# Performance work log

Measured on AMD Instinct MI355X. Metric: run time of the kernel, lower is better.

The kernel has to match this reference:

```python
import jax, jax.numpy as jnp
import numpy as np

D_MODEL = 1024
NUM_HEADS = 16
THETA = 10000.0


def setup_inputs() -> dict:
    key = jax.random.key(0)
    ks = jax.random.split(key, 5)
    B, S, DM = 4, 2048, D_MODEL
    std = 2.0 / (DM + DM)
    return {
        "x": jax.random.normal(ks[0], (B, S, DM), dtype=jnp.float32),
        "w_q": jax.random.normal(ks[1], (DM, DM), dtype=jnp.float32) * std,
        "w_k": jax.random.normal(ks[2], (DM, DM), dtype=jnp.float32) * std,
        "w_v": jax.random.normal(ks[3], (DM, DM), dtype=jnp.float32) * std,
        "w_o": jax.random.normal(ks[4], (DM, DM), dtype=jnp.float32) * std,
        "token_positions": jnp.arange(S, dtype=jnp.int64 if jax.config.jax_enable_x64 else jnp.int32),
    }


def _apply_rope(t, pos, d_k):
    # t: (b, h, s, d_k); pos: (s,)
    half = d_k // 2
    k = jnp.arange(half, dtype=jnp.float32)
    inv_freq = THETA ** (-2.0 * k / d_k)          # (half,)
    ang = pos.astype(jnp.float32)[:, None] * inv_freq  # (s, half)
    cos, sin = jnp.cos(ang), jnp.sin(ang)
    xe = t[..., 0::2]  # (b, h, s, half)
    xo = t[..., 1::2]
    re = cos * xe - sin * xo
    ro = sin * xe + cos * xo
    return jnp.stack([re, ro], axis=-1).reshape(t.shape)


def reference(x, w_q, w_k, w_v, w_o, token_positions):
    B, S, DM = x.shape
    H = NUM_HEADS
    d = DM // H
    # projections: x @ W.T, W is (h*d, d_model)
    def proj(w):
        y = jnp.einsum('bsm,em->bse', x, w)
        return y.reshape(B, S, H, d).transpose(0, 2, 1, 3)  # (b, h, s, d)
    q, k, v = proj(w_q), proj(w_k), proj(w_v)
    q = _apply_rope(q, token_positions, d)
    k = _apply_rope(k, token_positions, d)
    scale = 1.0 / jnp.sqrt(jnp.float32(d))
    scores = jnp.einsum('bhqd,bhkd->bhqk', q, k) * scale  # (b, h, s, s)
    causal = jnp.tril(jnp.ones((S, S), dtype=bool))
    scores = jnp.where(causal, scores, -jnp.inf)
    attn = jax.nn.softmax(scores, axis=-1)
    out = jnp.einsum('bhqk,bhkd->bhqd', attn, v)
    out = out.transpose(0, 2, 1, 3).reshape(B, S, DM)
    return jnp.einsum('bse,oe->bso', out, w_o)
```

## Files before the change

### kernel.cpp

```cpp
#include <hip/hip_runtime.h>
#include <hip/hip_bf16.h>

typedef __attribute__((ext_vector_type(8))) __bf16 bf16x8;
typedef __attribute__((ext_vector_type(2))) __bf16 bf16x2;
typedef __attribute__((ext_vector_type(2))) float f32x2;
typedef __attribute__((ext_vector_type(4))) float f32x4;
typedef __attribute__((ext_vector_type(16))) float f32x16;
typedef __attribute__((ext_vector_type(4))) unsigned int u32x4;
typedef __attribute__((ext_vector_type(2))) int i32x2;

#define MFMA16 __builtin_amdgcn_mfma_f32_16x16x32_bf16
#define MFMA32 __builtin_amdgcn_mfma_f32_32x32x16_bf16
#define GLOAD_LDS(g, l)                                                      \
  __builtin_amdgcn_global_load_lds(                                          \
      (const __attribute__((address_space(1))) void*)(g),                    \
      (__attribute__((address_space(3))) void*)(l), 16, 0, 0)

static __device__ __forceinline__ unsigned short f2bf(float f) {
  return __builtin_bit_cast(unsigned short, (__bf16)f);
}
static __device__ __forceinline__ unsigned int cvt2(float a, float b) {
  f32x2 t = {a, b};
  return __builtin_bit_cast(unsigned int, __builtin_convertvector(t, bf16x2));
}

__global__ __launch_bounds__(256) void cast_bf16_k(const float* __restrict__ in,
                                                   unsigned short* __restrict__ out,
                                                   int n8) {
  int i = blockIdx.x * 256 + threadIdx.x;
  if (i >= n8) return;
  const float4* p = (const float4*)in + (size_t)i * 2;
  float4 a = p[0], b = p[1];
  uint4 r;
  r.x = cvt2(a.x, a.y); r.y = cvt2(a.z, a.w);
  r.z = cvt2(b.x, b.y); r.w = cvt2(b.z, b.w);
  *((uint4*)out + i) = r;
}

__global__ __launch_bounds__(256) void rope_tab_k(const int* __restrict__ pos,
                                                  float2* __restrict__ tab) {
  int t = blockIdx.x * 256 + threadIdx.x;
  int s = t >> 5, k = t & 31;
  float p = (float)pos[s];
  float inv = powf(10000.0f, -(float)(2 * k) / 64.0f);
  float ang = p * inv;
  tab[t] = make_float2(cosf(ang), sinf(ang));
}

template <int MODE>
__global__ __launch_bounds__(256) void gemm_bt(
    const unsigned short* __restrict__ A, const unsigned short* __restrict__ W,
    unsigned short* __restrict__ Qb, unsigned short* __restrict__ Kb,
    unsigned short* __restrict__ Vb, float* __restrict__ Cout,
    const float2* __restrict__ rtab) {
  __shared__ unsigned short As[128 * 64];
  __shared__ unsigned short Bs[128 * 64];
  const int tid = threadIdx.x;
  const int lane = tid & 63;
  const int w = tid >> 6;
  const int wr = w >> 1, wc = w & 1;
  const int hi = lane >> 4, lo = lane & 15;
  const int m0 = blockIdx.x * 128;
  const int n0 = blockIdx.y * 128;
  const int z = blockIdx.z;
  const unsigned short* Bmat = W + (size_t)z * 1024 * 1024;

  const int sr = lane >> 3;
  const int sc8 = (lane & 7) * 8;

  f32x4 acc[4][4] = {};

  for (int kt = 0; kt < 16; ++kt) {
    const int kofs = kt * 64;
#pragma unroll
    for (int c = 0; c < 4; ++c) {
      const int rowA = c * 32 + w * 8;
      const unsigned short* ga = A + (size_t)(m0 + rowA + sr) * 1024 + kofs + sc8;
      GLOAD_LDS(ga, &As[rowA * 64]);
      const unsigned short* gb = Bmat + (size_t)(n0 + rowA + sr) * 1024 + kofs + sc8;
      GLOAD_LDS(gb, &Bs[rowA * 64]);
    }
    __syncthreads();
#pragma unroll
    for (int kb = 0; kb < 2; ++kb) {
      bf16x8 af[4], bfr[4];
#pragma unroll
      for (int mt = 0; mt < 4; ++mt)
        af[mt] = *(const bf16x8*)&As[(wr * 64 + mt * 16 + lo) * 64 + kb * 32 + hi * 8];
#pragma unroll
      for (int nt = 0; nt < 4; ++nt)
        bfr[nt] = *(const bf16x8*)&Bs[(wc * 64 + nt * 16 + lo) * 64 + kb * 32 + hi * 8];
#pragma unroll
      for (int mt = 0; mt < 4; ++mt)
#pragma unroll
        for (int nt = 0; nt < 4; ++nt)
          acc[mt][nt] = MFMA16(af[mt], bfr[nt], acc[mt][nt], 0, 0, 0);
    }
    __syncthreads();
  }

#pragma unroll
  for (int mt = 0; mt < 4; ++mt) {
#pragma unroll
    for (int nt = 0; nt < 4; ++nt) {
      const int c = n0 + wc * 64 + nt * 16 + lo;
#pragma unroll
      for (int j = 0; j < 4; ++j) {
        const int r = m0 + wr * 64 + mt * 16 + hi * 4 + j;
        float v = acc[mt][nt][j];
        if constexpr (MODE == 1) {
          Cout[(size_t)r * 1024 + c] = v;
        } else if constexpr (MODE == 2) {
          Vb[(size_t)r * 8192 + c] = f2bf(v);
        } else {
          const float other = __shfl_xor(v, 1);
          const int b = r >> 11, s = r & 2047;
          const int h = c >> 6, dd = c & 63;
          float2 cs = rtab[s * 32 + (dd >> 1)];
          float outv = (dd & 1) ? (cs.y * other + cs.x * v)
                                : (cs.x * v - cs.y * other);
          if (z == 0) outv *= 0.18033688012f;
          unsigned short* dst = (z == 0) ? Qb : Kb;
          dst[((size_t)(b * 16 + h) * 2048 + s) * 64 + dd] = f2bf(outv);
        }
      }
    }
  }
}

__global__ __launch_bounds__(256) void attn_k(const unsigned short* __restrict__ Qb,
                                              const unsigned short* __restrict__ Kb,
                                              const unsigned short* __restrict__ VtG,
                                              unsigned short* __restrict__ Ob) {
  __shared__ unsigned short Kl[2][64 * 64];
  __shared__ unsigned short Vl[2][64 * 64];
  const int tid = threadIdx.x;
  const int lane = tid & 63;
  const int w = tid >> 6;
  const int q32 = lane & 31;
  const int hi = lane >> 5;
  const int l7 = lane & 7;
  const int lin = blockIdx.x;
  const int slot = lin >> 3;
  const int bh = (lin & 7) * 8 + (slot >> 3);
  const int p = slot & 7;
  const int b = bh >> 4, h = bh & 15;
  const unsigned short* Qp = Qb + (size_t)bh * 2048 * 64;
  const unsigned short* Kp = Kb + (size_t)bh * 2048 * 64;
  const unsigned short* Vg = VtG + (size_t)h * 64 * 8192 + b * 2048;

  const int srow = lane >> 3;
  const int csrc = l7 ^ srow;

  auto stage = [&](int kt, int buf) {
#pragma unroll
    for (int i = 0; i < 2; ++i) {
      const int r = w * 16 + i * 8 + srow;
      GLOAD_LDS(Kp + ((size_t)(kt * 64 + r)) * 64 + csrc * 8,
                &Kl[buf][(w * 16 + i * 8) * 64]);
      GLOAD_LDS(Vg + (size_t)r * 8192 + kt * 64 + csrc * 8,
                &Vl[buf][(w * 16 + i * 8) * 64]);
    }
  };

  for (int phase = 0; phase < 2; ++phase) {
    const int qt = phase ? p : 15 - p;
    const int qw = qt * 128 + w * 32;
    const int qpos = qw + q32;

    bf16x8 qf[4];
#pragma unroll
    for (int ds = 0; ds < 4; ++ds)
      qf[ds] = *(const bf16x8*)&Qp[(size_t)qpos * 64 + ds * 16 + hi * 8];

    f32x16 oa0 = {}, oa1 = {};
    float mrow = -1e30f, lsum = 0.0f;
    const int ntiles = 2 * qt + 2;

    stage(0, 0);
    asm volatile("s_waitcnt vmcnt(0)" ::: "memory");
    __builtin_amdgcn_s_barrier();
    asm volatile("" ::: "memory");

    int cur = 0;
    for (int kt = 0; kt < ntiles; ++kt) {
      if (kt + 1 < ntiles) stage(kt + 1, cur ^ 1);
      const unsigned short* Kc = &Kl[cur][0];
      const unsigned short* Vc = &Vl[cur][0];

      f32x16 s0 = {}, s1 = {};
#pragma unroll
      for (int ds = 0; ds < 4; ++ds) {
        const int cc = ((ds * 2 + hi) ^ l7) * 8;
        bf16x8 k0 = *(const bf16x8*)&Kc[q32 * 64 + cc];
        bf16x8 k1 = *(const bf16x8*)&Kc[(32 + q32) * 64 + cc];
        s0 = MFMA32(k0, qf[ds], s0, 0, 0, 0);
        s1 = MFMA32(k1, qf[ds], s1, 0, 0, 0);
      }

      if (kt * 64 + 63 > qw) {
#pragma unroll
        for (int r = 0; r < 16; ++r) {
          const int krel = (r & 3) + 8 * (r >> 2) + 4 * hi;
          if (kt * 64 + krel > qpos) s0[r] = -1e30f;
          if (kt * 64 + 32 + krel > qpos) s1[r] = -1e30f;
        }
      }

      float tmax = -1e30f;
#pragma unroll
      for (int r = 0; r < 16; ++r) tmax = fmaxf(tmax, fmaxf(s0[r], s1[r]));
      tmax = fmaxf(tmax, __shfl_xor(tmax, 32));
      if (!__all(tmax - mrow <= 8.0f)) {
        const float mnew = fmaxf(mrow, tmax);
        const float alpha = exp2f(mrow - mnew);
        mrow = mnew;
        lsum *= alpha;
#pragma unroll
        for (int r = 0; r < 16; ++r) { oa0[r] *= alpha; oa1[r] *= alpha; }
      }
      float rsum = 0.0f;
#pragma unroll
      for (int r = 0; r < 16; ++r) {
        s0[r] = exp2f(s0[r] - mrow);
        s1[r] = exp2f(s1[r] - mrow);
        rsum += s0[r] + s1[r];
      }
      rsum += __shfl_xor(rsum, 32);
      lsum += rsum;

      unsigned int A0[8], A1[8];
#pragma unroll
      for (int i = 0; i < 8; ++i) {
        A0[i] = cvt2(s0[2 * i], s0[2 * i + 1]);
        A1[i] = cvt2(s1[2 * i], s1[2 * i + 1]);
      }
      i32x2 r02 = __builtin_amdgcn_permlane32_swap((int)A0[0], (int)A0[2], 0, 0);
      i32x2 r13 = __builtin_amdgcn_permlane32_swap((int)A0[1], (int)A0[3], 0, 0);
      i32x2 r46 = __builtin_amdgcn_permlane32_swap((int)A0[4], (int)A0[6], 0, 0);
      i32x2 r57 = __builtin_amdgcn_permlane32_swap((int)A0[5], (int)A0[7], 0, 0);
      i32x2 t02 = __builtin_amdgcn_permlane32_swap((int)A1[0], (int)A1[2], 0, 0);
      i32x2 t13 = __builtin_amdgcn_permlane32_swap((int)A1[1], (int)A1[3], 0, 0);
      i32x2 t46 = __builtin_amdgcn_permlane32_swap((int)A1[4], (int)A1[6], 0, 0);
      i32x2 t57 = __builtin_amdgcn_permlane32_swap((int)A1[5], (int)A1[7], 0, 0);
      const u32x4 pw0 = {(unsigned)r02[0], (unsigned)r13[0], (unsigned)r02[1], (unsigned)r13[1]};
      const u32x4 pw1 = {(unsigned)r46[0], (unsigned)r57[0], (unsigned)r46[1], (unsigned)r57[1]};
      const u32x4 pw2 = {(unsigned)t02[0], (unsigned)t13[0], (unsigned)t02[1], (unsigned)t13[1]};
      const u32x4 pw3 = {(unsigned)t46[0], (unsigned)t57[0], (unsigned)t46[1], (unsigned)t57[1]};

#pragma unroll
      for (int ks = 0; ks < 4; ++ks) {
        const int cc = ((ks * 2 + hi) ^ l7) * 8;
        bf16x8 v0 = *(const bf16x8*)&Vc[q32 * 64 + cc];
        bf16x8 v1 = *(const bf16x8*)&Vc[(32 + q32) * 64 + cc];
        const u32x4 pwk = (ks == 0) ? pw0 : (ks == 1) ? pw1 : (ks == 2) ? pw2 : pw3;
        bf16x8 pb = __builtin_bit_cast(bf16x8, pwk);
        oa0 = MFMA32(v0, pb, oa0, 0, 0, 0);
        oa1 = MFMA32(v1, pb, oa1, 0, 0, 0);
      }

      asm volatile("s_waitcnt vmcnt(0)" ::: "memory");
      __builtin_amdgcn_s_barrier();
      asm volatile("" ::: "memory");
      cur ^= 1;
    }

    const float invl = 1.0f / lsum;
    unsigned short* orow = Ob + ((size_t)(b * 2048 + qpos)) * 1024 + h * 64;
#pragma unroll
    for (int g = 0; g < 4; ++g) {
      uint2 o0, o1;
      o0.x = cvt2(oa0[4 * g + 0] * invl, oa0[4 * g + 1] * invl);
      o0.y = cvt2(oa0[4 * g + 2] * invl, oa0[4 * g + 3] * invl);
      o1.x = cvt2(oa1[4 * g + 0] * invl, oa1[4 * g + 1] * invl);
      o1.y = cvt2(oa1[4 * g + 2] * invl, oa1[4 * g + 3] * invl);
      *(uint2*)&orow[g * 8 + hi * 4] = o0;
      *(uint2*)&orow[32 + g * 8 + hi * 4] = o1;
    }
  }
}

extern "C" void kernel_launch(void* const* d_in, const int* in_sizes, int n_in,
                              void* d_out, int out_size, void* d_ws, size_t ws_size,
                              hipStream_t stream) {
  const float* x  = (const float*)d_in[0];
  const float* wq = (const float*)d_in[1];
  const float* wk = (const float*)d_in[2];
  const float* wv = (const float*)d_in[3];
  const float* wo = (const float*)d_in[4];
  const int* pos  = (const int*)d_in[5];

  char* ws = (char*)d_ws;
  unsigned short* xb  = (unsigned short*)(ws);
  unsigned short* wb  = (unsigned short*)(ws + 16777216);
  unsigned short* Qb  = (unsigned short*)(ws + 25165824);
  unsigned short* Kb  = (unsigned short*)(ws + 41943040);
  unsigned short* Vt  = (unsigned short*)(ws + 58720256);
  unsigned short* Ob  = (unsigned short*)(ws + 75497472);
  float2* tab         = (float2*)(ws + 92274688);

  cast_bf16_k<<<4096, 256, 0, stream>>>(x, xb, 1048576);
  cast_bf16_k<<<512, 256, 0, stream>>>(wq, wb + 0 * 1048576, 131072);
  cast_bf16_k<<<512, 256, 0, stream>>>(wk, wb + 1 * 1048576, 131072);
  cast_bf16_k<<<512, 256, 0, stream>>>(wv, wb + 2 * 1048576, 131072);
  cast_bf16_k<<<512, 256, 0, stream>>>(wo, wb + 3 * 1048576, 131072);
  rope_tab_k<<<256, 256, 0, stream>>>(pos, tab);
  gemm_bt<0><<<dim3(64, 8, 2), 256, 0, stream>>>(xb, wb, Qb, Kb, nullptr, nullptr, tab);
  gemm_bt<2><<<dim3(8, 64, 1), 256, 0, stream>>>(wb + 2 * 1048576, xb, nullptr,
                                                 nullptr, Vt, nullptr, tab);
  attn_k<<<dim3(512), 256, 0, stream>>>(Qb, Kb, Vt, Ob);
  gemm_bt<1><<<dim3(64, 8, 1), 256, 0, stream>>>(Ob, wb + 3 * 1048576, nullptr,
                                                 nullptr, nullptr, (float*)d_out, tab);
}
```

Before: 305.7 us.

## Switch projection GEMM to 32x32 MFMA with XOR-swizzled LDS layout

Replaces the 16x16x32 MFMA tiling in the projection/output GEMM with 32x32x16 MFMAs (four 32x32 accumulators per wave). The global-to-LDS loads now write chunks in an XOR-swizzled column order that matches the fragment reads, to avoid LDS bank conflicts. The aim is fewer LDS fragment reads per MFMA and higher MFMA throughput. The epilogue row mapping is rewritten to follow the 32x32 accumulator layout.

```diff
diff --git a/kernel.cpp b/kernel.cpp
--- a/kernel.cpp
+++ b/kernel.cpp
@@ -4,12 +4,10 @@
 typedef __attribute__((ext_vector_type(8))) __bf16 bf16x8;
 typedef __attribute__((ext_vector_type(2))) __bf16 bf16x2;
 typedef __attribute__((ext_vector_type(2))) float f32x2;
-typedef __attribute__((ext_vector_type(4))) float f32x4;
 typedef __attribute__((ext_vector_type(16))) float f32x16;
 typedef __attribute__((ext_vector_type(4))) unsigned int u32x4;
 typedef __attribute__((ext_vector_type(2))) int i32x2;
 
-#define MFMA16 __builtin_amdgcn_mfma_f32_16x16x32_bf16
 #define MFMA32 __builtin_amdgcn_mfma_f32_32x32x16_bf16
 #define GLOAD_LDS(g, l)                                                      \
   __builtin_amdgcn_global_load_lds(                                          \
@@ -59,62 +57,63 @@
   const int lane = tid & 63;
   const int w = tid >> 6;
   const int wr = w >> 1, wc = w & 1;
-  const int hi = lane >> 4, lo = lane & 15;
+  const int q32 = lane & 31;
+  const int hi = lane >> 5;
+  const int l7 = lane & 7;
   const int m0 = blockIdx.x * 128;
   const int n0 = blockIdx.y * 128;
   const int z = blockIdx.z;
   const unsigned short* Bmat = W + (size_t)z * 1024 * 1024;
 
   const int sr = lane >> 3;
-  const int sc8 = (lane & 7) * 8;
-
-  f32x4 acc[4][4] = {};
+  const int csrc = l7 ^ sr;
+
+  f32x16 acc00 = {}, acc01 = {}, acc10 = {}, acc11 = {};
 
   for (int kt = 0; kt < 16; ++kt) {
     const int kofs = kt * 64;
 #pragma unroll
     for (int c = 0; c < 4; ++c) {
       const int rowA = c * 32 + w * 8;
-      const unsigned short* ga = A + (size_t)(m0 + rowA + sr) * 1024 + kofs + sc8;
-      GLOAD_LDS(ga, &As[rowA * 64]);
-      const unsigned short* gb = Bmat + (size_t)(n0 + rowA + sr) * 1024 + kofs + sc8;
-      GLOAD_LDS(gb, &Bs[rowA * 64]);
+      GLOAD_LDS(A + (size_t)(m0 + rowA + sr) * 1024 + kofs + csrc * 8,
+                &As[rowA * 64]);
+      GLOAD_LDS(Bmat + (size_t)(n0 + rowA + sr) * 1024 + kofs + csrc * 8,
+                &Bs[rowA * 64]);
     }
     __syncthreads();
 #pragma unroll
-    for (int kb = 0; kb < 2; ++kb) {
-      bf16x8 af[4], bfr[4];
-#pragma unroll
-      for (int mt = 0; mt < 4; ++mt)
-        af[mt] = *(const bf16x8*)&As[(wr * 64 + mt * 16 + lo) * 64 + kb * 32 + hi * 8];
-#pragma unroll
-      for (int nt = 0; nt < 4; ++nt)
-        bfr[nt] = *(const bf16x8*)&Bs[(wc * 64 + nt * 16 + lo) * 64 + kb * 32 + hi * 8];
-#pragma unroll
-      for (int mt = 0; mt < 4; ++mt)
-#pragma unroll
-        for (int nt = 0; nt < 4; ++nt)
-          acc[mt][nt] = MFMA16(af[mt], bfr[nt], acc[mt][nt], 0, 0, 0);
+    for (int kk = 0; kk < 4; ++kk) {
+      const int cc = ((kk * 2 + hi) ^ l7) * 8;
+      bf16x8 a0 = *(const bf16x8*)&As[(wr * 64 + q32) * 64 + cc];
+      bf16x8 a1 = *(const bf16x8*)&As[(wr * 64 + 32 + q32) * 64 + cc];
+      bf16x8 b0 = *(const bf16x8*)&Bs[(wc * 64 + q32) * 64 + cc];
+      bf16x8 b1 = *(const bf16x8*)&Bs[(wc * 64 + 32 + q32) * 64 + cc];
+      acc00 = MFMA32(a0, b0, acc00, 0, 0, 0);
+      acc01 = MFMA32(a0, b1, acc01, 0, 0, 0);
+      acc10 = MFMA32(a1, b0, acc10, 0, 0, 0);
+      acc11 = MFMA32(a1, b1, acc11, 0, 0, 0);
     }
     __syncthreads();
   }
 
 #pragma unroll
-  for (int mt = 0; mt < 4; ++mt) {
-#pragma unroll
-    for (int nt = 0; nt < 4; ++nt) {
-      const int c = n0 + wc * 64 + nt * 16 + lo;
-#pragma unroll
-      for (int j = 0; j < 4; ++j) {
-        const int r = m0 + wr * 64 + mt * 16 + hi * 4 + j;
-        float v = acc[mt][nt][j];
+  for (int mt = 0; mt < 2; ++mt) {
+#pragma unroll
+    for (int nt = 0; nt < 2; ++nt) {
+      const f32x16 av = (mt == 0) ? (nt == 0 ? acc00 : acc01)
+                                  : (nt == 0 ? acc10 : acc11);
+      const int c = n0 + wc * 64 + nt * 32 + q32;
+#pragma unroll
+      for (int r = 0; r < 16; ++r) {
+        const int rr = m0 + wr * 64 + mt * 32 + (r & 3) + 8 * (r >> 2) + 4 * hi;
+        float v = av[r];
         if constexpr (MODE == 1) {
-          Cout[(size_t)r * 1024 + c] = v;
+          Cout[(size_t)rr * 1024 + c] = v;
         } else if constexpr (MODE == 2) {
-          Vb[(size_t)r * 8192 + c] = f2bf(v);
+          Vb[(size_t)rr * 8192 + c] = f2bf(v);
         } else {
           const float other = __shfl_xor(v, 1);
-          const int b = r >> 11, s = r & 2047;
+          const int b = rr >> 11, s = rr & 2047;
           const int h = c >> 6, dd = c & 63;
           float2 cs = rtab[s * 32 + (dd >> 1)];
           float outv = (dd & 1) ? (cs.y * other + cs.x * v)
```

Result: faster. 283.8 us (-7.2%).
